# Kernel optimization log

Measured on AMD Instinct MI355X. Metric: run time of the kernel, lower is better.

Reference implementation:

```python
import jax, jax.numpy as jnp
import numpy as np

B, S, D, H = 1, 4096, 1024, 16
HD = D // H  # head_size = 64

def setup_inputs() -> dict:
    key = jax.random.key(0)
    ks = jax.random.split(key, 9)
    scale = 1.0 / np.sqrt(D)
    return {
        "x": jax.random.normal(ks[0], (B, S, D), jnp.float32),
        "Wq": jax.random.normal(ks[1], (D, D), jnp.float32) * scale,
        "bq": jax.random.normal(ks[2], (D,), jnp.float32) * 0.01,
        "Wk": jax.random.normal(ks[3], (D, D), jnp.float32) * scale,
        "bk": jax.random.normal(ks[4], (D,), jnp.float32) * 0.01,
        "Wv": jax.random.normal(ks[5], (D, D), jnp.float32) * scale,
        "bv": jax.random.normal(ks[6], (D,), jnp.float32) * 0.01,
        "Wo": jax.random.normal(ks[7], (D, D), jnp.float32) * scale,
        "bo": jax.random.normal(ks[8], (D,), jnp.float32) * 0.01,
    }

def _split_heads(t):
    # (B, S, D) -> (B, H, S, HD)
    return t.reshape(B, S, H, HD).transpose(0, 2, 1, 3)

def reference(x, Wq, bq, Wk, bk, Wv, bv, Wo, bo):
    q = _split_heads(x @ Wq + bq)
    k = _split_heads(x @ Wk + bk)
    v = _split_heads(x @ Wv + bv)
    # scores: (B, H, S, S), materialized as in the original naive attention
    scores = jnp.einsum('bhqd,bhkd->bhqk', q, k) / jnp.sqrt(jnp.asarray(HD, q.dtype))
    causal = jnp.tril(jnp.ones((S, S), dtype=bool))  # tril mask, broadcast over (B, H)
    scores = jnp.where(causal[None, None], scores, jnp.asarray(-1e9, scores.dtype))
    attn = jax.nn.softmax(scores, axis=-1)
    out = jnp.einsum('bhqk,bhkd->bhqd', attn, v)  # (B, H, S, HD)
    out = out.transpose(0, 2, 1, 3).reshape(B, S, D)  # combine heads
    return out @ Wo + bo
```

## Files before the change

### kernel.cpp

```cpp
#include <hip/hip_runtime.h>

#define SEQ 4096
#define DM  1024
#define NH  16
#define HDIM 64

typedef unsigned short u16;
typedef unsigned int   u32;
typedef __bf16 bf16x8 __attribute__((ext_vector_type(8)));
typedef float f32x4 __attribute__((ext_vector_type(4)));

__device__ __forceinline__ float bf2f(u16 u) {
    unsigned v = ((unsigned)u) << 16;
    float f;
    __builtin_memcpy(&f, &v, 4);
    return f;
}
__device__ __forceinline__ u16 f2bf(float f) {
    unsigned u;
    __builtin_memcpy(&u, &f, 4);
    return (u16)((u + 0x7fffu + ((u >> 16) & 1u)) >> 16);
}
__device__ __forceinline__ u32 bfpack(float a, float b) {
    u32 ua, ub;
    __builtin_memcpy(&ua, &a, 4);
    __builtin_memcpy(&ub, &b, 4);
    return ((ua + 0x8000u) >> 16) | ((ub + 0x8000u) & 0xffff0000u);
}

typedef const __attribute__((address_space(1))) unsigned int gas_uint;
typedef __attribute__((address_space(3))) unsigned int las_uint;
__device__ __forceinline__ void gld16(const u16* g, u16* l) {
    __builtin_amdgcn_global_load_lds((gas_uint*)g, (las_uint*)l, 16, 0, 0);
}

__device__ __forceinline__ f32x4 mfma16(bf16x8 a, bf16x8 b, f32x4 c) {
    return __builtin_amdgcn_mfma_f32_16x16x32_bf16(a, b, c, 0, 0, 0);
}

#define QSCALE 0.18033688011f

__global__ __launch_bounds__(256) void detect_k(const u16* __restrict__ w,
                                                int* __restrict__ flags) {
    __shared__ float red[256];
    const int t = threadIdx.x;
    float mx = 0.f;
    for (int i = t; i < 4096; i += 256) {
        float v = fabsf(bf2f(w[i]));
        if (v < 3e38f) mx = fmaxf(mx, v);
    }
    red[t] = mx;
    __syncthreads();
    for (int s = 128; s > 0; s >>= 1) {
        if (t < s) red[t] = fmaxf(red[t], red[t + s]);
        __syncthreads();
    }
    if (t == 0) {
        flags[0] = (red[0] > 1e4f) ? 1 : 0;
        flags[1] = 0;
    }
}

__global__ __launch_bounds__(256) void prep_w(const void* w0, const void* w1,
                                              const void* w2, const void* w3,
                                              const void* b0, const void* b1,
                                              const void* b2, const void* b3,
                                              u16* __restrict__ wt,
                                              u16* __restrict__ b_dst,
                                              const int* __restrict__ flags) {
    __shared__ u16 tile[32][33];
    const int f = flags[0];
    const int z = blockIdx.z;
    const void* win[4] = {w0, w1, w2, w3};
    const void* bin[4] = {b0, b1, b2, b3};
    const void* in = win[z];
    u16* out = wt + (size_t)z * DM * DM;
    const float scale = (z == 0) ? QSCALE : 1.0f;

    const int bx = blockIdx.x * 32;
    const int by = blockIdx.y * 32;
    const int tx = threadIdx.x & 31;
    const int ty = threadIdx.x >> 5;
#pragma unroll
    for (int i = ty; i < 32; i += 8) {
        size_t idx = (size_t)(by + i) * DM + bx + tx;
        float v = f ? ((const float*)in)[idx] : bf2f(((const u16*)in)[idx]);
        tile[i][tx] = f2bf(v * scale);
    }
    __syncthreads();
#pragma unroll
    for (int i = ty; i < 32; i += 8) out[(size_t)(bx + i) * DM + by + tx] = tile[tx][i];

    if (blockIdx.x == 0 && blockIdx.y == 0) {
        const void* bi = bin[z];
        for (int i = threadIdx.x; i < DM; i += 256) {
            float v = f ? ((const float*)bi)[i] : bf2f(((const u16*)bi)[i]);
            b_dst[z * DM + i] = f2bf(v * scale);
        }
    }
}

__global__ __launch_bounds__(256) void cvt_x8(const void* __restrict__ src,
                                              u16* __restrict__ dst,
                                              const int* __restrict__ flags) {
    const size_t i = ((size_t)blockIdx.x * 256 + threadIdx.x) * 8;
    if (flags[0]) {
        const float4* s4 = (const float4*)((const float*)src + i);
        float4 a = s4[0], b = s4[1];
        uint4 o;
        o.x = bfpack(a.x, a.y);
        o.y = bfpack(a.z, a.w);
        o.z = bfpack(b.x, b.y);
        o.w = bfpack(b.z, b.w);
        *(uint4*)(dst + i) = o;
    } else {
        *(uint4*)(dst + i) = *(const uint4*)((const u16*)src + i);
    }
}

__global__ __launch_bounds__(256, 2) void gemm128(const u16* __restrict__ A,
                                                  const u16* __restrict__ Bt,
                                                  const u16* __restrict__ bias,
                                                  void* __restrict__ C,
                                                  int M, int N, int K,
                                                  const int* __restrict__ flags) {
    __shared__ u16 As[128 * 32];
    __shared__ u16 Bs[128 * 32];
    const int f    = flags[0];
    const int tid  = threadIdx.x;
    const int lane = tid & 63;
    const int w    = tid >> 6;
    const int m    = lane & 15;
    const int quad = lane >> 4;
    const int wr   = w >> 1;
    const int wc   = w & 1;
    const int mb = blockIdx.x * 128;
    const int nb = blockIdx.y * 128;

    f32x4 acc[4][4] = {};

    for (int kb = 0; kb < K; kb += 32) {
        __syncthreads();
#pragma unroll
        for (int i = 0; i < 2; ++i) {
            const int Lb = i * 256 + w * 64;
            const int L  = Lb + lane;
            const int row = L >> 2, cb = L & 3;
            gld16(&A[(size_t)(mb + row) * K + kb + cb * 8], &As[Lb * 8]);
            gld16(&Bt[(size_t)(nb + row) * K + kb + cb * 8], &Bs[Lb * 8]);
        }
        __syncthreads();

        bf16x8 af[4];
#pragma unroll
        for (int mt = 0; mt < 4; ++mt)
            af[mt] = *(const bf16x8*)&As[(wr * 64 + mt * 16 + m) * 32 + quad * 8];
#pragma unroll
        for (int ct = 0; ct < 4; ++ct) {
            bf16x8 bfr = *(const bf16x8*)&Bs[(wc * 64 + ct * 16 + m) * 32 + quad * 8];
#pragma unroll
            for (int mt = 0; mt < 4; ++mt)
                acc[mt][ct] = mfma16(af[mt], bfr, acc[mt][ct]);
        }
    }

#pragma unroll
    for (int ct = 0; ct < 4; ++ct) {
        float bv = bf2f(bias[nb + wc * 64 + ct * 16 + m]);
#pragma unroll
        for (int mt = 0; mt < 4; ++mt) {
#pragma unroll
            for (int r = 0; r < 4; ++r) {
                int row = mb + wr * 64 + mt * 16 + quad * 4 + r;
                size_t idx = (size_t)row * N + nb + wc * 64 + ct * 16 + m;
                float v = acc[mt][ct][r] + bv;
                if (f) ((float*)C)[idx] = v;
                else   ((u16*)C)[idx]   = f2bf(v);
            }
        }
    }
}

__global__ __launch_bounds__(256) void vt_k(const u16* __restrict__ qkv,
                                            u16* __restrict__ Vt) {
    __shared__ u16 T[64][72];
    const int st = blockIdx.x;
    const int h  = blockIdx.y;
    const int t  = threadIdx.x;
    const int sl = t >> 2, c = t & 3;
    const u16* src = &qkv[(size_t)(st * 64 + sl) * 3072 + 2048 + h * 64 + c * 16];
    *(uint4*)&T[sl][c * 16]     = *(const uint4*)src;
    *(uint4*)&T[sl][c * 16 + 8] = *(const uint4*)(src + 8);
    __syncthreads();
    const int dl = t >> 2, c2 = t & 3;
    u16 tmp[16];
#pragma unroll
    for (int i = 0; i < 16; ++i) tmp[i] = T[c2 * 16 + i][dl];
    u16* dst = &Vt[(size_t)(h * 64 + dl) * SEQ + st * 64 + c2 * 16];
    *(uint4*)dst       = *(const uint4*)&tmp[0];
    *(uint4*)(dst + 8) = *(const uint4*)&tmp[8];
}

__global__ __launch_bounds__(256, 2) void attn_split(const u16* __restrict__ QKV,
                                                     const u16* __restrict__ Vt,
                                                     u16* __restrict__ ab,
                                                     u16* __restrict__ slotB,
                                                     float* __restrict__ lA,
                                                     float* __restrict__ lB) {
    __shared__ u16 Ks[2][64 * 64];
    __shared__ u16 Vs[2][64 * 64];

    const int tid  = threadIdx.x;
    const int lane = tid & 63;
    const int w    = tid >> 6;
    const int m    = lane & 15;
    const int quad = lane >> 4;
    const int l3   = lane >> 3;
    const int cx   = ((lane & 7) ^ l3) * 8;
    const int m7   = m & 7;

    const int b = blockIdx.x;
    const int x = b & 7;
    const int u = b >> 3;
    int qt2, head, half;
    if (u < 32) { qt2 = 15 - (u >> 1); head = 2 * x + (u & 1);        half = 0; }
    else        { int u2 = u - 32; qt2 = u2 >> 1; head = 2 * x + (u2 & 1); half = 1; }
    const int hc  = head * HDIM;
    const int k0t = half ? 2 * qt2 + 2 : 0;
    const int k1t = half ? 4 * qt2 + 3 : 2 * qt2 + 1;
    const int qw  = qt2 * 256 + w * 64;
    const int dw  = qw >> 6;

    bf16x8 qf[4][2];
#pragma unroll
    for (int qt4 = 0; qt4 < 4; ++qt4)
#pragma unroll
        for (int c = 0; c < 2; ++c)
            qf[qt4][c] = *(const bf16x8*)&QKV[(size_t)(qw + qt4 * 16 + m) * 3072 + hc + c * 32 + quad * 8];

    f32x4 o_acc[4][4] = {};
    float l_part[4] = {0.f, 0.f, 0.f, 0.f};

#pragma unroll
    for (int i = 0; i < 2; ++i) {
        const int r = w * 16 + i * 8 + l3;
        gld16(&QKV[(size_t)(k0t * 64 + r) * 3072 + 1024 + hc + cx], &Ks[0][(w * 16 + i * 8) * 64]);
        gld16(&Vt[(size_t)(hc + r) * SEQ + k0t * 64 + cx],           &Vs[0][(w * 16 + i * 8) * 64]);
    }

    for (int kt = k0t; kt <= k1t; ++kt) {
        const int cur = (kt - k0t) & 1;
        __syncthreads();

        if (kt < k1t) {
            const int nb = 1 - cur;
            const int nkt = kt + 1;
#pragma unroll
            for (int i = 0; i < 2; ++i) {
                const int r = w * 16 + i * 8 + l3;
                gld16(&QKV[(size_t)(nkt * 64 + r) * 3072 + 1024 + hc + cx], &Ks[nb][(w * 16 + i * 8) * 64]);
                gld16(&Vt[(size_t)(hc + r) * SEQ + nkt * 64 + cx],           &Vs[nb][(w * 16 + i * 8) * 64]);
            }
        }

        if (kt > dw) continue;

        const u16* ksb = Ks[cur];
        const u16* vsb = Vs[cur];

#pragma unroll
        for (int st = 0; st < 4; ++st) {
            bf16x8 kf[2];
#pragma unroll
            for (int c = 0; c < 2; ++c)
                kf[c] = *(const bf16x8*)&ksb[(st * 16 + m) * 64 + (((c * 4 + quad) ^ m7) * 8)];

            f32x4 sc[4];
#pragma unroll
            for (int qt4 = 0; qt4 < 4; ++qt4) {
                f32x4 a = {};
                a = mfma16(kf[0], qf[qt4][0], a);
                a = mfma16(kf[1], qf[qt4][1], a);
                sc[qt4] = a;
            }

            if (kt == dw) {
#pragma unroll
                for (int qt4 = 0; qt4 < 4; ++qt4)
#pragma unroll
                    for (int r = 0; r < 4; ++r) {
                        float p = __builtin_amdgcn_exp2f(sc[qt4][r]);
                        sc[qt4][r] = (st * 16 + quad * 4 + r > qt4 * 16 + m) ? 0.f : p;
                    }
            } else {
#pragma unroll
                for (int qt4 = 0; qt4 < 4; ++qt4)
#pragma unroll
                    for (int r = 0; r < 4; ++r)
                        sc[qt4][r] = __builtin_amdgcn_exp2f(sc[qt4][r]);
            }

#pragma unroll
            for (int qt4 = 0; qt4 < 4; ++qt4)
                l_part[qt4] += sc[qt4][0] + sc[qt4][1] + sc[qt4][2] + sc[qt4][3];

            bf16x8 pa[4];
#pragma unroll
            for (int qt4 = 0; qt4 < 4; ++qt4) {
                uint4 t;
                t.x = bfpack(sc[qt4][0], sc[qt4][1]);
                t.y = bfpack(sc[qt4][2], sc[qt4][3]);
                t.z = 0; t.w = 0;
                __builtin_memcpy(&pa[qt4], &t, 16);
            }

#pragma unroll
            for (int dt = 0; dt < 4; ++dt) {
                const int chx = ((2 * st + (quad >> 1)) ^ m7);
                uint2 v2 = *(const uint2*)&vsb[(dt * 16 + m) * 64 + chx * 8 + (quad & 1) * 4];
                uint4 t;
                t.x = v2.x; t.y = v2.y; t.z = 0; t.w = 0;
                bf16x8 vf;
                __builtin_memcpy(&vf, &t, 16);
#pragma unroll
                for (int qt4 = 0; qt4 < 4; ++qt4)
                    o_acc[qt4][dt] = mfma16(pa[qt4], vf, o_acc[qt4][dt]);
            }
        }
    }

#pragma unroll
    for (int qt4 = 0; qt4 < 4; ++qt4) {
        l_part[qt4] += __shfl_xor(l_part[qt4], 16, 64);
        l_part[qt4] += __shfl_xor(l_part[qt4], 32, 64);
    }

    u16*   dst = half ? slotB : ab;
    float* lb  = half ? lB : lA;
#pragma unroll
    for (int qt4 = 0; qt4 < 4; ++qt4)
#pragma unroll
        for (int dt = 0; dt < 4; ++dt)
#pragma unroll
            for (int r = 0; r < 4; ++r) {
                int row = qw + qt4 * 16 + quad * 4 + r;
                dst[(size_t)row * DM + hc + dt * 16 + m] = f2bf(o_acc[qt4][dt][r]);
            }
    if (lane < 16) {
#pragma unroll
        for (int qt4 = 0; qt4 < 4; ++qt4)
            lb[head * SEQ + qw + qt4 * 16 + lane] = l_part[qt4];
    }
}

__global__ __launch_bounds__(256) void merge_k(u16* __restrict__ ab,
                                               const u16* __restrict__ sB,
                                               const float* __restrict__ lA,
                                               const float* __restrict__ lB) {
    const int gid = blockIdx.x * 256 + threadIdx.x;
    const int rl = gid >> 7;
    const int cg = gid & 127;
    const int h  = cg >> 3;
    const float inv = 1.0f / (lA[h * SEQ + rl] + lB[h * SEQ + rl]);
    uint4 va = *(const uint4*)(ab + (size_t)rl * DM + cg * 8);
    uint4 vb = *(const uint4*)(sB + (size_t)rl * DM + cg * 8);
    const u16* a16 = (const u16*)&va;
    const u16* b16 = (const u16*)&vb;
    u16 oo[8];
#pragma unroll
    for (int i = 0; i < 8; ++i) oo[i] = f2bf((bf2f(a16[i]) + bf2f(b16[i])) * inv);
    *(uint4*)(ab + (size_t)rl * DM + cg * 8) = *(const uint4*)&oo[0];
}

extern "C" void kernel_launch(void* const* d_in, const int* in_sizes, int n_in,
                              void* d_out, int out_size, void* d_ws, size_t ws_size,
                              hipStream_t stream) {
    (void)in_sizes; (void)n_in; (void)out_size; (void)ws_size;

    u16* ws    = (u16*)d_ws;
    int* flags = (int*)d_ws;
    u16* xc    = ws + 64;
    u16* Vt_g  = xc;
    u16* Wtqkv = xc + (size_t)SEQ * DM;
    u16* Wto   = Wtqkv + (size_t)3 * DM * DM;
    u16* bqkv  = Wto + (size_t)DM * DM;
    u16* boc   = bqkv + 3 * DM;
    u16* qkv   = boc + DM;
    u16* ab    = qkv + (size_t)SEQ * 3 * DM;
    u16* slotB = ab + (size_t)SEQ * DM;
    float* lAf = (float*)Wtqkv;
    float* lBf = lAf + NH * SEQ;

    detect_k<<<1, 256, 0, stream>>>((const u16*)d_in[1], flags);

    prep_w<<<dim3(DM / 32, DM / 32, 4), 256, 0, stream>>>(
        d_in[1], d_in[3], d_in[5], d_in[7],
        d_in[2], d_in[4], d_in[6], d_in[8],
        Wtqkv, bqkv, flags);

    cvt_x8<<<SEQ * DM / 2048, 256, 0, stream>>>(d_in[0], xc, flags);

    gemm128<<<dim3(SEQ / 128, 3 * DM / 128), 256, 0, stream>>>(
        xc, Wtqkv, bqkv, qkv, SEQ, 3 * DM, DM, flags + 1);

    vt_k<<<dim3(SEQ / 64, NH), 256, 0, stream>>>(qkv, Vt_g);

    attn_split<<<dim3(512), 256, 0, stream>>>(qkv, Vt_g, ab, slotB, lAf, lBf);

    merge_k<<<dim3(SEQ * 128 / 256), 256, 0, stream>>>(ab, slotB, lAf, lBf);

    gemm128<<<dim3(SEQ / 128, DM / 128), 256, 0, stream>>>(
        ab, Wto, boc, d_out, SEQ, DM, DM, flags);
}
```

Baseline: 243.5 us.

## Split causal attention KV range three ways and use full-K PV MFMA

Attention work is split into three KV partitions per query tile instead of two, which launches 768 blocks with occupancy hint 3, and a three-way merge combines the partial results. The PV product now packs two 16-key score slices into one full bf16x8 MFMA operand instead of zero-padding half of it, halving the PV MFMA count. The QKV GEMM writes Q, K and V to separate contiguous buffers, and V's buffer is reused as the third partial slot. Risks are the extra merge traffic and register pressure under the higher occupancy bound.

```diff
diff --git a/kernel.cpp b/kernel.cpp
--- a/kernel.cpp
+++ b/kernel.cpp
@@ -121,7 +121,9 @@
 __global__ __launch_bounds__(256, 2) void gemm128(const u16* __restrict__ A,
                                                   const u16* __restrict__ Bt,
                                                   const u16* __restrict__ bias,
-                                                  void* __restrict__ C,
+                                                  void* __restrict__ C0,
+                                                  void* __restrict__ C1,
+                                                  void* __restrict__ C2,
                                                   int M, int N, int K,
                                                   const int* __restrict__ flags) {
     __shared__ u16 As[128 * 32];
@@ -136,6 +138,9 @@
     const int wc   = w & 1;
     const int mb = blockIdx.x * 128;
     const int nb = blockIdx.y * 128;
+    const int mat = nb >> 10;
+    const int lnb = nb & 1023;
+    void* C = (mat == 0) ? C0 : ((mat == 1) ? C1 : C2);
 
     f32x4 acc[4][4] = {};
 
@@ -172,7 +177,7 @@
 #pragma unroll
             for (int r = 0; r < 4; ++r) {
                 int row = mb + wr * 64 + mt * 16 + quad * 4 + r;
-                size_t idx = (size_t)row * N + nb + wc * 64 + ct * 16 + m;
+                size_t idx = (size_t)row * DM + lnb + wc * 64 + ct * 16 + m;
                 float v = acc[mt][ct][r] + bv;
                 if (f) ((float*)C)[idx] = v;
                 else   ((u16*)C)[idx]   = f2bf(v);
@@ -181,14 +186,14 @@
     }
 }
 
-__global__ __launch_bounds__(256) void vt_k(const u16* __restrict__ qkv,
+__global__ __launch_bounds__(256) void vt_k(const u16* __restrict__ V,
                                             u16* __restrict__ Vt) {
     __shared__ u16 T[64][72];
     const int st = blockIdx.x;
     const int h  = blockIdx.y;
     const int t  = threadIdx.x;
     const int sl = t >> 2, c = t & 3;
-    const u16* src = &qkv[(size_t)(st * 64 + sl) * 3072 + 2048 + h * 64 + c * 16];
+    const u16* src = &V[(size_t)(st * 64 + sl) * DM + h * 64 + c * 16];
     *(uint4*)&T[sl][c * 16]     = *(const uint4*)src;
     *(uint4*)&T[sl][c * 16 + 8] = *(const uint4*)(src + 8);
     __syncthreads();
@@ -201,12 +206,15 @@
     *(uint4*)(dst + 8) = *(const uint4*)&tmp[8];
 }
 
-__global__ __launch_bounds__(256, 2) void attn_split(const u16* __restrict__ QKV,
+__global__ __launch_bounds__(256, 3) void attn_split(const u16* __restrict__ Qb,
+                                                     const u16* __restrict__ Kb,
                                                      const u16* __restrict__ Vt,
-                                                     u16* __restrict__ ab,
-                                                     u16* __restrict__ slotB,
-                                                     float* __restrict__ lA,
-                                                     float* __restrict__ lB) {
+                                                     u16* __restrict__ slot0,
+                                                     u16* __restrict__ slot1,
+                                                     u16* __restrict__ slot2,
+                                                     float* __restrict__ l0,
+                                                     float* __restrict__ l1,
+                                                     float* __restrict__ l2) {
     __shared__ u16 Ks[2][64 * 64];
     __shared__ u16 Vs[2][64 * 64];
 
@@ -219,24 +227,27 @@
     const int cx   = ((lane & 7) ^ l3) * 8;
     const int m7   = m & 7;
 
-    const int b = blockIdx.x;
-    const int x = b & 7;
-    const int u = b >> 3;
-    int qt2, head, half;
-    if (u < 32) { qt2 = 15 - (u >> 1); head = 2 * x + (u & 1);        half = 0; }
-    else        { int u2 = u - 32; qt2 = u2 >> 1; head = 2 * x + (u2 & 1); half = 1; }
-    const int hc  = head * HDIM;
-    const int k0t = half ? 2 * qt2 + 2 : 0;
-    const int k1t = half ? 4 * qt2 + 3 : 2 * qt2 + 1;
-    const int qw  = qt2 * 256 + w * 64;
-    const int dw  = qw >> 6;
+    const int b    = blockIdx.x;
+    const int x    = b & 7;
+    const int u    = b >> 3;
+    const int qt2  = 15 - (u / 6);
+    const int v6   = u % 6;
+    const int head = 2 * x + (v6 / 3);
+    const int part = v6 % 3;
+    const int hc   = head * HDIM;
+    const int n    = 4 * qt2 + 4;
+    const int k0t  = part * n / 3;
+    const int k1t  = (part + 1) * n / 3 - 1;
+
+    const int qw = qt2 * 256 + w * 64;
+    const int dw = qw >> 6;
 
     bf16x8 qf[4][2];
 #pragma unroll
     for (int qt4 = 0; qt4 < 4; ++qt4)
 #pragma unroll
         for (int c = 0; c < 2; ++c)
-            qf[qt4][c] = *(const bf16x8*)&QKV[(size_t)(qw + qt4 * 16 + m) * 3072 + hc + c * 32 + quad * 8];
+            qf[qt4][c] = *(const bf16x8*)&Qb[(size_t)(qw + qt4 * 16 + m) * DM + hc + c * 32 + quad * 8];
 
     f32x4 o_acc[4][4] = {};
     float l_part[4] = {0.f, 0.f, 0.f, 0.f};
@@ -244,8 +255,8 @@
 #pragma unroll
     for (int i = 0; i < 2; ++i) {
         const int r = w * 16 + i * 8 + l3;
-        gld16(&QKV[(size_t)(k0t * 64 + r) * 3072 + 1024 + hc + cx], &Ks[0][(w * 16 + i * 8) * 64]);
-        gld16(&Vt[(size_t)(hc + r) * SEQ + k0t * 64 + cx],           &Vs[0][(w * 16 + i * 8) * 64]);
+        gld16(&Kb[(size_t)(k0t * 64 + r) * DM + hc + cx], &Ks[0][(w * 16 + i * 8) * 64]);
+        gld16(&Vt[(size_t)(hc + r) * SEQ + k0t * 64 + cx], &Vs[0][(w * 16 + i * 8) * 64]);
     }
 
     for (int kt = k0t; kt <= k1t; ++kt) {
@@ -253,13 +264,13 @@
         __syncthreads();
 
         if (kt < k1t) {
-            const int nb = 1 - cur;
+            const int nbf = 1 - cur;
             const int nkt = kt + 1;
 #pragma unroll
             for (int i = 0; i < 2; ++i) {
                 const int r = w * 16 + i * 8 + l3;
-                gld16(&QKV[(size_t)(nkt * 64 + r) * 3072 + 1024 + hc + cx], &Ks[nb][(w * 16 + i * 8) * 64]);
-                gld16(&Vt[(size_t)(hc + r) * SEQ + nkt * 64 + cx],           &Vs[nb][(w * 16 + i * 8) * 64]);
+                gld16(&Kb[(size_t)(nkt * 64 + r) * DM + hc + cx], &Ks[nbf][(w * 16 + i * 8) * 64]);
+                gld16(&Vt[(size_t)(hc + r) * SEQ + nkt * 64 + cx], &Vs[nbf][(w * 16 + i * 8) * 64]);
             }
         }
 
@@ -269,57 +280,65 @@
         const u16* vsb = Vs[cur];
 
 #pragma unroll
-        for (int st = 0; st < 4; ++st) {
-            bf16x8 kf[2];
-#pragma unroll
-            for (int c = 0; c < 2; ++c)
-                kf[c] = *(const bf16x8*)&ksb[(st * 16 + m) * 64 + (((c * 4 + quad) ^ m7) * 8)];
-
-            f32x4 sc[4];
-#pragma unroll
-            for (int qt4 = 0; qt4 < 4; ++qt4) {
-                f32x4 a = {};
-                a = mfma16(kf[0], qf[qt4][0], a);
-                a = mfma16(kf[1], qf[qt4][1], a);
-                sc[qt4] = a;
+        for (int p = 0; p < 2; ++p) {
+            uint4 pa_raw[4];
+
+#pragma unroll
+            for (int stt = 0; stt < 2; ++stt) {
+                const int st = 2 * p + stt;
+                bf16x8 kf[2];
+#pragma unroll
+                for (int c = 0; c < 2; ++c)
+                    kf[c] = *(const bf16x8*)&ksb[(st * 16 + m) * 64 + (((c * 4 + quad) ^ m7) * 8)];
+
+                f32x4 sc[4];
+#pragma unroll
+                for (int qt4 = 0; qt4 < 4; ++qt4) {
+                    f32x4 a = {};
+                    a = mfma16(kf[0], qf[qt4][0], a);
+                    a = mfma16(kf[1], qf[qt4][1], a);
+                    sc[qt4] = a;
+                }
+
+                if (kt == dw) {
+#pragma unroll
+                    for (int qt4 = 0; qt4 < 4; ++qt4)
+#pragma unroll
+                        for (int r = 0; r < 4; ++r) {
+                            float pp = __builtin_amdgcn_exp2f(sc[qt4][r]);
+                            sc[qt4][r] = (st * 16 + quad * 4 + r > qt4 * 16 + m) ? 0.f : pp;
+                        }
+                } else {
+#pragma unroll
+                    for (int qt4 = 0; qt4 < 4; ++qt4)
+#pragma unroll
+                        for (int r = 0; r < 4; ++r)
+                            sc[qt4][r] = __builtin_amdgcn_exp2f(sc[qt4][r]);
+                }
+
+#pragma unroll
+                for (int qt4 = 0; qt4 < 4; ++qt4) {
+                    l_part[qt4] += sc[qt4][0] + sc[qt4][1] + sc[qt4][2] + sc[qt4][3];
+                    const u32 pk0 = bfpack(sc[qt4][0], sc[qt4][1]);
+                    const u32 pk1 = bfpack(sc[qt4][2], sc[qt4][3]);
+                    if (stt == 0) { pa_raw[qt4].x = pk0; pa_raw[qt4].y = pk1; }
+                    else          { pa_raw[qt4].z = pk0; pa_raw[qt4].w = pk1; }
+                }
             }
 
-            if (kt == dw) {
-#pragma unroll
-                for (int qt4 = 0; qt4 < 4; ++qt4)
-#pragma unroll
-                    for (int r = 0; r < 4; ++r) {
-                        float p = __builtin_amdgcn_exp2f(sc[qt4][r]);
-                        sc[qt4][r] = (st * 16 + quad * 4 + r > qt4 * 16 + m) ? 0.f : p;
-                    }
-            } else {
-#pragma unroll
-                for (int qt4 = 0; qt4 < 4; ++qt4)
-#pragma unroll
-                    for (int r = 0; r < 4; ++r)
-                        sc[qt4][r] = __builtin_amdgcn_exp2f(sc[qt4][r]);
-            }
-
-#pragma unroll
-            for (int qt4 = 0; qt4 < 4; ++qt4)
-                l_part[qt4] += sc[qt4][0] + sc[qt4][1] + sc[qt4][2] + sc[qt4][3];
-
             bf16x8 pa[4];
 #pragma unroll
-            for (int qt4 = 0; qt4 < 4; ++qt4) {
+            for (int qt4 = 0; qt4 < 4; ++qt4) __builtin_memcpy(&pa[qt4], &pa_raw[qt4], 16);
+
+#pragma unroll
+            for (int dt = 0; dt < 4; ++dt) {
+                const int base = (dt * 16 + m) * 64;
+                const int clo = ((4 * p + (quad >> 1)) ^ m7) * 8 + (quad & 1) * 4;
+                const int chi = ((4 * p + 2 + (quad >> 1)) ^ m7) * 8 + (quad & 1) * 4;
+                uint2 vlo = *(const uint2*)&vsb[base + clo];
+                uint2 vhi = *(const uint2*)&vsb[base + chi];
                 uint4 t;
-                t.x = bfpack(sc[qt4][0], sc[qt4][1]);
-                t.y = bfpack(sc[qt4][2], sc[qt4][3]);
-                t.z = 0; t.w = 0;
-                __builtin_memcpy(&pa[qt4], &t, 16);
-            }
-
-#pragma unroll
-            for (int dt = 0; dt < 4; ++dt) {
-                const int chx = ((2 * st + (quad >> 1)) ^ m7);
-                uint2 v2 = *(const uint2*)&vsb[(dt * 16 + m) * 64 + chx * 8 + (quad & 1) * 4];
-                uint4 t;
-                t.x = v2.x; t.y = v2.y; t.z = 0; t.w = 0;
+                t.x = vlo.x; t.y = vlo.y; t.z = vhi.x; t.w = vhi.y;
                 bf16x8 vf;
                 __builtin_memcpy(&vf, &t, 16);
 #pragma unroll
@@ -335,8 +354,8 @@
         l_part[qt4] += __shfl_xor(l_part[qt4], 32, 64);
     }
 
-    u16*   dst = half ? slotB : ab;
-    float* lb  = half ? lB : lA;
+    u16*   dst = (part == 0) ? slot0 : ((part == 1) ? slot1 : slot2);
+    float* lb  = (part == 0) ? l0 : ((part == 1) ? l1 : l2);
 #pragma unroll
     for (int qt4 = 0; qt4 < 4; ++qt4)
 #pragma unroll
@@ -353,23 +372,28 @@
     }
 }
 
-__global__ __launch_bounds__(256) void merge_k(u16* __restrict__ ab,
-                                               const u16* __restrict__ sB,
-                                               const float* __restrict__ lA,
-                                               const float* __restrict__ lB) {
+__global__ __launch_bounds__(256) void merge_k(u16* __restrict__ s0,
+                                               const u16* __restrict__ s1,
+                                               const u16* __restrict__ s2,
+                                               const float* __restrict__ l0,
+                                               const float* __restrict__ l1,
+                                               const float* __restrict__ l2) {
     const int gid = blockIdx.x * 256 + threadIdx.x;
     const int rl = gid >> 7;
     const int cg = gid & 127;
     const int h  = cg >> 3;
-    const float inv = 1.0f / (lA[h * SEQ + rl] + lB[h * SEQ + rl]);
-    uint4 va = *(const uint4*)(ab + (size_t)rl * DM + cg * 8);
-    uint4 vb = *(const uint4*)(sB + (size_t)rl * DM + cg * 8);
+    const float inv = 1.0f / (l0[h * SEQ + rl] + l1[h * SEQ + rl] + l2[h * SEQ + rl]);
+    uint4 va = *(const uint4*)(s0 + (size_t)rl * DM + cg * 8);
+    uint4 vb = *(const uint4*)(s1 + (size_t)rl * DM + cg * 8);
+    uint4 vc = *(const uint4*)(s2 + (size_t)rl * DM + cg * 8);
     const u16* a16 = (const u16*)&va;
     const u16* b16 = (const u16*)&vb;
+    const u16* c16 = (const u16*)&vc;
     u16 oo[8];
 #pragma unroll
-    for (int i = 0; i < 8; ++i) oo[i] = f2bf((bf2f(a16[i]) + bf2f(b16[i])) * inv);
-    *(uint4*)(ab + (size_t)rl * DM + cg * 8) = *(const uint4*)&oo[0];
+    for (int i = 0; i < 8; ++i)
+        oo[i] = f2bf((bf2f(a16[i]) + bf2f(b16[i]) + bf2f(c16[i])) * inv);
+    *(uint4*)(s0 + (size_t)rl * DM + cg * 8) = *(const uint4*)&oo[0];
 }
 
 extern "C" void kernel_launch(void* const* d_in, const int* in_sizes, int n_in,
@@ -385,11 +409,15 @@
     u16* Wto   = Wtqkv + (size_t)3 * DM * DM;
     u16* bqkv  = Wto + (size_t)DM * DM;
     u16* boc   = bqkv + 3 * DM;
-    u16* qkv   = boc + DM;
-    u16* ab    = qkv + (size_t)SEQ * 3 * DM;
+    u16* Qb    = boc + DM;
+    u16* Kb    = Qb + (size_t)SEQ * DM;
+    u16* Vb    = Kb + (size_t)SEQ * DM;
+    u16* ab    = Vb + (size_t)SEQ * DM;
     u16* slotB = ab + (size_t)SEQ * DM;
-    float* lAf = (float*)Wtqkv;
-    float* lBf = lAf + NH * SEQ;
+    u16* slotC = Vb;
+    float* l0f = (float*)Wtqkv;
+    float* l1f = l0f + NH * SEQ;
+    float* l2f = l1f + NH * SEQ;
 
     detect_k<<<1, 256, 0, stream>>>((const u16*)d_in[1], flags);
 
@@ -401,14 +429,15 @@
     cvt_x8<<<SEQ * DM / 2048, 256, 0, stream>>>(d_in[0], xc, flags);
 
     gemm128<<<dim3(SEQ / 128, 3 * DM / 128), 256, 0, stream>>>(
-        xc, Wtqkv, bqkv, qkv, SEQ, 3 * DM, DM, flags + 1);
-
-    vt_k<<<dim3(SEQ / 64, NH), 256, 0, stream>>>(qkv, Vt_g);
-
-    attn_split<<<dim3(512), 256, 0, stream>>>(qkv, Vt_g, ab, slotB, lAf, lBf);
-
-    merge_k<<<dim3(SEQ * 128 / 256), 256, 0, stream>>>(ab, slotB, lAf, lBf);
+        xc, Wtqkv, bqkv, Qb, Kb, Vb, SEQ, 3 * DM, DM, flags + 1);
+
+    vt_k<<<dim3(SEQ / 64, NH), 256, 0, stream>>>(Vb, Vt_g);
+
+    attn_split<<<dim3(768), 256, 0, stream>>>(Qb, Kb, Vt_g, ab, slotB, slotC,
+                                              l0f, l1f, l2f);
+
+    merge_k<<<dim3(SEQ * 128 / 256), 256, 0, stream>>>(ab, slotB, slotC, l0f, l1f, l2f);
 
     gemm128<<<dim3(SEQ / 128, DM / 128), 256, 0, stream>>>(
-        ab, Wto, boc, d_out, SEQ, DM, DM, flags);
-}
+        ab, Wto, boc, d_out, d_out, d_out, SEQ, DM, DM, flags);
+}
```

New measurement: 319.3 us. +31.1%, slower.
